# Optimization experiments

Measured on AMD Instinct MI355X. Metric: run time of the kernel, lower is better.

The kernel has to match this reference:

```python
import jax, jax.numpy as jnp
import numpy as np

B, S, D = 2, 2048, 2048          # batch, seq_len, model_dim
H, HD, RD, L = 16, 128, 64, 512  # heads, head_dim, rope_dim, latent_dim


def _rope_cos_sin(seq_len, dim, dtype):
    inv_freq = 1.0 / (10000.0 ** (jnp.arange(0, dim, 2, dtype=jnp.float32) / dim))
    freqs = jnp.outer(jnp.arange(seq_len, dtype=jnp.float32), inv_freq)  # [S, dim/2]
    emb = jnp.concatenate([freqs, freqs], axis=-1)                        # [S, dim]
    return jnp.cos(emb).astype(dtype), jnp.sin(emb).astype(dtype)


def _rotate_half(x):
    x1, x2 = jnp.split(x, 2, axis=-1)
    return jnp.concatenate([-x2, x1], axis=-1)


def _apply_rope(q, k):
    # q, k: [B, S, H, rope_dim]
    cos, sin = _rope_cos_sin(q.shape[1], q.shape[-1], q.dtype)
    cos = cos[None, :, None, :]
    sin = sin[None, :, None, :]
    return q * cos + _rotate_half(q) * sin, k * cos + _rotate_half(k) * sin


def setup_inputs() -> dict:
    key = jax.random.key(0)
    ks = jax.random.split(key, 6)
    x = jax.random.normal(ks[0], (B, S, D), dtype=jnp.float32)
    mask = jnp.tril(jnp.ones((1, 1, S, S), dtype=jnp.bool_))  # causal
    s = lambda fan_in: 1.0 / np.sqrt(fan_in)
    w_kv_down = jax.random.normal(ks[1], (D, L), jnp.float32) * s(D)
    w_kv_up = jax.random.normal(ks[2], (L, H * (2 * HD + RD)), jnp.float32) * s(L)
    w_q_down = jax.random.normal(ks[3], (D, L), jnp.float32) * s(D)
    w_q_up = jax.random.normal(ks[4], (L, H * (HD + RD)), jnp.float32) * s(L)
    w_o = jax.random.normal(ks[5], (H * HD, D), jnp.float32) * s(H * HD)
    return dict(x=x, mask=mask, w_kv_down=w_kv_down, w_kv_up=w_kv_up,
                w_q_down=w_q_down, w_q_up=w_q_up, w_o=w_o)


def reference(x, mask, w_kv_down, w_kv_up, w_q_down, w_q_up, w_o):
    b, s, _ = x.shape
    # low-rank KV path
    kv_full = (x @ w_kv_down @ w_kv_up).reshape(b, s, H, 2 * HD + RD)
    k_content = kv_full[..., :HD]
    k_rope = kv_full[..., HD:HD + RD]
    v = kv_full[..., HD + RD:]                     # [b, s, H, HD]
    # low-rank Q path
    q_full = (x @ w_q_down @ w_q_up).reshape(b, s, H, HD + RD)
    q_content = q_full[..., :HD]
    q_rope = q_full[..., HD:]
    # partial RoPE on the rope slice only
    q_rope, k_rope = _apply_rope(q_rope, k_rope)
    q = jnp.concatenate([q_content, q_rope], axis=-1)  # [b, s, H, HD+RD]
    k = jnp.concatenate([k_content, k_rope], axis=-1)
    scale = 1.0 / np.sqrt(HD + RD)
    scores = jnp.einsum('bqhd,bkhd->bhqk', q, k) * scale
    scores = jnp.where(mask, scores, jnp.finfo(scores.dtype).min)
    attn = jax.nn.softmax(scores, axis=-1)          # dropout_p=0.0 -> identity
    context = jnp.einsum('bhqk,bkhd->bqhd', attn, v).reshape(b, s, H * HD)
    return context @ w_o
```

## Files before the change

### kernel.cpp

```cpp
#include <hip/hip_runtime.h>
#include <hip/hip_bf16.h>

#define B_ 2
#define S_ 2048
#define D_ 2048
#define H_ 16
#define HD_ 128
#define RD_ 64
#define L_ 512
#define BS_ (B_ * S_)
#define KVH 320
#define QH 192

typedef unsigned short u16;
typedef __bf16 bf16x8 __attribute__((ext_vector_type(8)));
typedef float f32x4 __attribute__((ext_vector_type(4)));
typedef float f32x16 __attribute__((ext_vector_type(16)));
typedef unsigned short us8 __attribute__((ext_vector_type(8)));
typedef unsigned short us4 __attribute__((ext_vector_type(4)));

#define MFMA16(A, B, C) __builtin_amdgcn_mfma_f32_16x16x32_bf16((A), (B), (C), 0, 0, 0)
#define MFMA32(A, B, C) __builtin_amdgcn_mfma_f32_32x32x16_bf16((A), (B), (C), 0, 0, 0)

__device__ __forceinline__ u16 f2bf(float f) {
    unsigned int u = __builtin_bit_cast(unsigned int, f);
    u += 0x7FFFu + ((u >> 16) & 1u);
    return (u16)(u >> 16);
}
__device__ __forceinline__ float bf2f(u16 u) {
    unsigned int x = ((unsigned int)u) << 16;
    return __builtin_bit_cast(float, x);
}
__device__ __forceinline__ void async16(const void* g, void* l) {
    __builtin_amdgcn_global_load_lds((void __attribute__((address_space(1)))*)g,
                                     (void __attribute__((address_space(3)))*)l, 16, 0, 0);
}
__device__ __forceinline__ int swz4(int row) { return (row + (row >> 2)) & 3; }
__device__ __forceinline__ unsigned int cvtpk_bf16(float lo, float hi) {
    unsigned int r;
    asm("v_cvt_pk_bf16_f32 %0, %1, %2" : "=v"(r) : "v"(lo), "v"(hi));
    return r;
}

__global__ __launch_bounds__(256) void conv_f32_bf16(const float* __restrict__ in,
                                                     u16* __restrict__ outp) {
    const int i = blockIdx.x * 256 + threadIdx.x;
    float4 v = *(const float4*)(in + (size_t)i * 4);
    us4 o; o[0] = f2bf(v.x); o[1] = f2bf(v.y); o[2] = f2bf(v.z); o[3] = f2bf(v.w);
    *(us4*)(outp + (size_t)i * 4) = o;
}

__global__ __launch_bounds__(256) void transpose_f32_bf16(const float* __restrict__ W,
                                                          u16* __restrict__ Wt,
                                                          int K, int N) {
    __shared__ float tile[32][33];
    const int t = threadIdx.x, tx = t & 31, ty = t >> 5;
    const int n0 = blockIdx.x * 32, k0 = blockIdx.y * 32;
#pragma unroll
    for (int r = 0; r < 4; r++)
        tile[ty + 8 * r][tx] = W[(size_t)(k0 + ty + 8 * r) * N + n0 + tx];
    __syncthreads();
#pragma unroll
    for (int r = 0; r < 4; r++)
        Wt[(size_t)(n0 + ty + 8 * r) * K + k0 + tx] = f2bf(tile[tx][ty + 8 * r]);
}

__global__ __launch_bounds__(256) void transpose_v(const u16* __restrict__ kvf,
                                                   u16* __restrict__ vtg) {
    __shared__ u16 tile[32][33];
    const int t = threadIdx.x, tx = t & 31, ty = t >> 5;
    const int bh = blockIdx.z, b = bh >> 4, h = bh & 15;
    const int s0 = blockIdx.x * 32, d0 = blockIdx.y * 32;
#pragma unroll
    for (int r = 0; r < 4; r++)
        tile[ty + 8 * r][tx] = kvf[(size_t)(b * S_ + s0 + ty + 8 * r) * (H_ * KVH) + h * KVH + QH + d0 + tx];
    __syncthreads();
#pragma unroll
    for (int r = 0; r < 4; r++)
        vtg[((size_t)bh * HD_ + d0 + ty + 8 * r) * S_ + s0 + tx] = tile[tx][ty + 8 * r];
}

__global__ __launch_bounds__(256) void rope_both(u16* __restrict__ qf,
                                                 u16* __restrict__ kvf) {
    const int idx = blockIdx.x * 256 + threadIdx.x;
    const int d = idx & 31;
    const int h = (idx >> 5) & (H_ - 1);
    const int s = (idx >> 9) & (S_ - 1);
    const int b = idx >> 20;
    const int stride = blockIdx.y ? KVH : QH;
    u16* buf = blockIdx.y ? kvf : qf;

    const float inv_freq = powf(10000.0f, -(float)d * (1.0f / 32.0f));
    const float ang = (float)s * inv_freq;
    const float c = cosf(ang), sn = sinf(ang);

    u16* p = buf + ((size_t)((b * S_ + s) * H_) + h) * stride + HD_ + d;
    const float x1 = bf2f(p[0]);
    const float x2 = bf2f(p[32]);
    p[0]  = f2bf(x1 * c - x2 * sn);
    p[32] = f2bf(x2 * c + x1 * sn);
}

template <int WM, int WN, int TM, int TN, bool OUT_F32>
__global__ __launch_bounds__(WM * WN * 64) void gemm_bf16(
    const u16* __restrict__ A, int lda,
    const u16* __restrict__ Bt, int ldb,
    void* __restrict__ Cv, int ldc, int K, float alpha) {
    constexpr int BMt = WM * TM * 16;
    constexpr int BNt = WN * TN * 16;
    constexpr int NW  = WM * WN;
    constexpr int CA  = BMt / 16;
    constexpr int CB  = BNt / 16;

    __shared__ u16 As[BMt * 32];
    __shared__ u16 Bs[BNt * 32];

    const int t = threadIdx.x, w = t >> 6, l = t & 63;
    const int quad = l >> 4, n16 = l & 15;
    const int wr = w / WN, wc = w % WN;
    const size_t m0 = (size_t)blockIdx.y * BMt;
    const size_t n0 = (size_t)blockIdx.x * BNt;
    const int rowc = l >> 2, sbp = l & 3;

    f32x4 acc[TM][TN];
#pragma unroll
    for (int i = 0; i < TM; i++)
#pragma unroll
        for (int j = 0; j < TN; j++) acc[i][j] = (f32x4){0.f, 0.f, 0.f, 0.f};

    for (int k0 = 0; k0 < K; k0 += 32) {
#pragma unroll
        for (int c = w; c < CA; c += NW) {
            const int row = c * 16 + rowc;
            const int colc = ((sbp - swz4(row)) & 3) * 8;
            async16(A + (m0 + row) * lda + k0 + colc, &As[c * 512 + l * 8]);
        }
#pragma unroll
        for (int c = w; c < CB; c += NW) {
            const int row = c * 16 + rowc;
            const int colc = ((sbp - swz4(row)) & 3) * 8;
            async16(Bt + (n0 + row) * ldb + k0 + colc, &Bs[c * 512 + l * 8]);
        }
        __syncthreads();

        bf16x8 af[TM], bfr[TN];
#pragma unroll
        for (int i = 0; i < TM; i++) {
            const int row = wr * TM * 16 + i * 16 + n16;
            af[i] = *(const bf16x8*)&As[row * 32 + ((quad + swz4(row)) & 3) * 8];
        }
#pragma unroll
        for (int j = 0; j < TN; j++) {
            const int row = wc * TN * 16 + j * 16 + n16;
            bfr[j] = *(const bf16x8*)&Bs[row * 32 + ((quad + swz4(row)) & 3) * 8];
        }
#pragma unroll
        for (int i = 0; i < TM; i++)
#pragma unroll
            for (int j = 0; j < TN; j++) acc[i][j] = MFMA16(af[i], bfr[j], acc[i][j]);
        __syncthreads();
    }

#pragma unroll
    for (int i = 0; i < TM; i++) {
#pragma unroll
        for (int j = 0; j < TN; j++) {
#pragma unroll
            for (int r = 0; r < 4; r++) {
                const size_t row = m0 + wr * TM * 16 + i * 16 + quad * 4 + r;
                const size_t col = n0 + wc * TN * 16 + j * 16 + n16;
                const float v = acc[i][j][r] * alpha;
                if (OUT_F32) ((float*)Cv)[row * ldc + col] = v;
                else         ((u16*)Cv)[row * ldc + col] = f2bf(v);
            }
        }
    }
}

__global__ __launch_bounds__(128, 2) void attn_mfma(const u16* __restrict__ qf,
                                                    const u16* __restrict__ kvf,
                                                    const u16* __restrict__ vtg,
                                                    u16* __restrict__ ctx) {
    __shared__ u16 Ks[2][3 * 32 * 64];
    __shared__ u16 Vs[128 * 32];

    const int t = threadIdx.x, w = t >> 6, lane = t & 63;
    const int l31 = lane & 31, hi = lane >> 5;

    const int wg = blockIdx.x;
    const int xcd = wg & 7, j = wg >> 3;
    const int bh = xcd + 8 * (j & 3);
    const int qt = 31 - (j >> 2);
    const int b = bh >> 4, h = bh & 15;
    const int Q0 = qt * 64;

    const u16* Kbase = kvf + (size_t)(b * S_) * (H_ * KVH) + h * KVH;
    const u16* Vbase = vtg + (size_t)bh * HD_ * S_;

    const int scol = ((lane & 7) ^ (lane >> 3)) * 8;
    const int krl  = lane >> 3;
    const int vrow = lane >> 2;
    const int vcol = ((lane & 3) ^ (vrow & 3)) * 8;

    int koff[12];
#pragma unroll
    for (int c = 0; c < 12; c++)
        koff[c] = (c >> 2) * 2048 + (((c & 3) * 16 + hi * 8) ^ ((l31 & 7) * 8));
    int voff[2][4];
#pragma unroll
    for (int s = 0; s < 2; s++)
#pragma unroll
        for (int dt = 0; dt < 4; dt++)
            voff[s][dt] = (dt * 32 + l31) * 32 + ((s * 16 + hi * 8) ^ ((l31 & 3) * 8));

    bf16x8 qfrag[12];
    {
        const u16* qr = qf + (size_t)(b * S_ + Q0 + w * 32 + l31) * (H_ * QH) + h * QH + hi * 8;
#pragma unroll
        for (int c = 0; c < 12; c++) qfrag[c] = *(const bf16x8*)(qr + c * 16);
    }
    asm volatile("" ::: "memory");

    f32x16 O[4];
#pragma unroll
    for (int i = 0; i < 4; i++)
#pragma unroll
        for (int r = 0; r < 16; r++) O[i][r] = 0.f;
    float lrun = 0.f;

    const int qg = Q0 + w * 32 + l31;
    const int qmaxw = Q0 + w * 32 + 31;
    const int nkt = 2 * qt + 2;

#define ISSUE_K(KT, BUF)                                                        \
    _Pragma("unroll")                                                           \
    for (int ch = w; ch < 12; ch += 2) {                                        \
        const int c3 = ch >> 2, kq = ch & 3;                                    \
        async16(Kbase + (size_t)((KT) * 32 + kq * 8 + krl) * (H_ * KVH)         \
                      + c3 * 64 + scol,                                         \
                &Ks[BUF][c3 * 2048 + kq * 512 + lane * 8]);                     \
    }
#define ISSUE_V(KT)                                                             \
    _Pragma("unroll")                                                           \
    for (int ch = w; ch < 8; ch += 2) {                                         \
        async16(Vbase + (size_t)(ch * 16 + vrow) * S_ + (KT) * 32 + vcol,       \
                &Vs[ch * 512 + lane * 8]);                                      \
    }

    ISSUE_K(0, 0);
    ISSUE_V(0);

    for (int kt = 0; kt < nkt; kt++) {
        const int cur = kt & 1;
        if (kt > 0) {
            asm volatile("s_barrier" ::: "memory");
            ISSUE_V(kt);
        }
        if (kt + 1 < nkt) {
            ISSUE_K(kt + 1, cur ^ 1);
            asm volatile("s_waitcnt vmcnt(10)" ::: "memory");
        } else {
            asm volatile("s_waitcnt vmcnt(4)" ::: "memory");
        }
        asm volatile("s_barrier" ::: "memory");

        const bool active = (kt * 32) <= qmaxw;
        bf16x8 pfrag[2];
        if (active) {
            f32x16 sA;
#pragma unroll
            for (int r = 0; r < 16; r++) sA[r] = 0.f;
            __builtin_amdgcn_s_setprio(1);
#pragma unroll
            for (int c = 0; c < 12; c++) {
                bf16x8 kf = *(const bf16x8*)&Ks[cur][koff[c] + l31 * 64];
                sA = MFMA32(kf, qfrag[c], sA);
            }
            __builtin_amdgcn_s_setprio(0);

            const bool diag = (kt * 32 + 31) > (Q0 + w * 32);
#pragma unroll
            for (int r = 0; r < 16; r++) {
                const int crow = (r & 3) + 8 * (r >> 2) + 4 * hi;
                float pa = exp2f(sA[r]);
                if (diag && (kt * 32 + crow > qg)) pa = 0.f;
                lrun += pa;
                sA[r] = pa;
            }

#pragma unroll
            for (int s = 0; s < 2; s++) {
                const int r0 = s * 8;
                unsigned int x0 = cvtpk_bf16(sA[r0 + 0], sA[r0 + 1]);
                unsigned int y0 = cvtpk_bf16(sA[r0 + 4], sA[r0 + 5]);
                unsigned int x1 = cvtpk_bf16(sA[r0 + 2], sA[r0 + 3]);
                unsigned int y1 = cvtpk_bf16(sA[r0 + 6], sA[r0 + 7]);
                asm volatile("v_permlane32_swap_b32 %0, %1" : "+v"(x0), "+v"(y0));
                asm volatile("v_permlane32_swap_b32 %0, %1" : "+v"(x1), "+v"(y1));
                union { unsigned int wv[4]; bf16x8 v; } u_;
                u_.wv[0] = x0; u_.wv[1] = x1; u_.wv[2] = y0; u_.wv[3] = y1;
                pfrag[s] = u_.v;
            }
        }

        if (kt + 1 < nkt) asm volatile("s_waitcnt vmcnt(6)" ::: "memory");
        else              asm volatile("s_waitcnt vmcnt(0)" ::: "memory");
        asm volatile("s_barrier" ::: "memory");

        if (active) {
            __builtin_amdgcn_s_setprio(1);
#pragma unroll
            for (int s = 0; s < 2; s++) {
#pragma unroll
                for (int dt = 0; dt < 4; dt++) {
                    bf16x8 vf = *(const bf16x8*)&Vs[voff[s][dt]];
                    O[dt] = MFMA32(pfrag[s], vf, O[dt]);
                }
            }
            __builtin_amdgcn_s_setprio(0);
        }
    }
#undef ISSUE_K
#undef ISSUE_V

    lrun += __shfl_xor(lrun, 32, 64);
    float inv_[16];
#pragma unroll
    for (int r = 0; r < 16; r++) {
        const int crow = (r & 3) + 8 * (r >> 2) + 4 * hi;
        inv_[r] = 1.0f / __shfl(lrun, crow, 64);
    }
#pragma unroll
    for (int dt = 0; dt < 4; dt++)
#pragma unroll
        for (int r = 0; r < 16; r++) {
            const int crow = (r & 3) + 8 * (r >> 2) + 4 * hi;
            const int qrow = Q0 + w * 32 + crow;
            ctx[(size_t)(b * S_ + qrow) * (H_ * HD_) + h * HD_ + dt * 32 + l31] =
                f2bf(O[dt][r] * inv_[r]);
        }
}

extern "C" void kernel_launch(void* const* d_in, const int* in_sizes, int n_in,
                              void* d_out, int out_size, void* d_ws, size_t ws_size,
                              hipStream_t stream) {
    const float* x         = (const float*)d_in[0];
    const float* w_kv_down = (const float*)d_in[2];
    const float* w_kv_up   = (const float*)d_in[3];
    const float* w_q_down  = (const float*)d_in[4];
    const float* w_q_up    = (const float*)d_in[5];
    const float* w_o       = (const float*)d_in[6];
    float* out = (float*)d_out;

    char* ws = (char*)d_ws;
    size_t off = 0;
    u16* xb      = (u16*)(ws + off); off += (size_t)BS_ * D_ * 2;
    u16* wdt     = (u16*)(ws + off); off += (size_t)1024 * D_ * 2;
    u16* wkvup_t = (u16*)(ws + off); off += (size_t)(H_ * KVH) * L_ * 2;
    u16* wqup_t  = (u16*)(ws + off); off += (size_t)(H_ * QH) * L_ * 2;
    u16* wo_t    = (u16*)(ws + off); off += (size_t)D_ * (H_ * HD_) * 2;
    u16* low     = (u16*)(ws + off); off += (size_t)BS_ * 1024 * 2;
    u16* kv_full = (u16*)(ws + off); off += (size_t)BS_ * H_ * KVH * 2;
    u16* q_full  = (u16*)(ws + off); off += (size_t)BS_ * H_ * QH * 2;
    u16* vtg     = (u16*)(ws + off); off += (size_t)B_ * H_ * HD_ * S_ * 2;
    u16* ctx     = (u16*)(ws + off); off += (size_t)BS_ * H_ * HD_ * 2;

    const float qscale = 1.442695041f / 13.856406461f;

    conv_f32_bf16<<<(BS_ * D_) / 1024, 256, 0, stream>>>(x, xb);
    transpose_f32_bf16<<<dim3(L_ / 32, D_ / 32), 256, 0, stream>>>(w_kv_down, wdt, D_, L_);
    transpose_f32_bf16<<<dim3(L_ / 32, D_ / 32), 256, 0, stream>>>(w_q_down, wdt + (size_t)512 * D_, D_, L_);
    transpose_f32_bf16<<<dim3((H_ * KVH) / 32, L_ / 32), 256, 0, stream>>>(w_kv_up, wkvup_t, L_, H_ * KVH);
    transpose_f32_bf16<<<dim3((H_ * QH) / 32, L_ / 32), 256, 0, stream>>>(w_q_up, wqup_t, L_, H_ * QH);
    transpose_f32_bf16<<<dim3(D_ / 32, (H_ * HD_) / 32), 256, 0, stream>>>(w_o, wo_t, H_ * HD_, D_);

    gemm_bf16<2, 2, 4, 2, false><<<dim3(1024 / 64, BS_ / 128), 256, 0, stream>>>(
        xb, D_, wdt, D_, low, 1024, D_, 1.0f);
    gemm_bf16<2, 2, 4, 4, false><<<dim3((H_ * KVH) / 128, BS_ / 128), 256, 0, stream>>>(
        low, 1024, wkvup_t, L_, kv_full, H_ * KVH, L_, 1.0f);
    gemm_bf16<2, 2, 4, 4, false><<<dim3((H_ * QH) / 128, BS_ / 128), 256, 0, stream>>>(
        low + 512, 1024, wqup_t, L_, q_full, H_ * QH, L_, qscale);

    rope_both<<<dim3((B_ * S_ * H_ * 32) / 256, 2), 256, 0, stream>>>(q_full, kv_full);

    transpose_v<<<dim3(S_ / 32, HD_ / 32, B_ * H_), 256, 0, stream>>>(kv_full, vtg);

    attn_mfma<<<dim3(1024), 128, 0, stream>>>(q_full, kv_full, vtg, ctx);

    gemm_bf16<2, 2, 4, 4, true><<<dim3(D_ / 128, BS_ / 128), 256, 0, stream>>>(
        ctx, D_, wo_t, D_, out, D_, D_, 1.0f);
}
```

Before: 416.6 us.

## Enlarge attention tiles to 128 queries with split-K waves and LDS reduction

The attention kernel now uses 512-thread workgroups that each cover 128 query rows and 64-key tiles. Two groups of four waves split each key tile into halves, and their partial outputs and row sums are combined through shared memory at the end. This increases K/V reuse per block and changes the ordering of query tiles to balance causal work. The cost is more shared memory, extra barriers and a final reduction, and half the waves are idle during the epilogue.

```diff
diff --git a/kernel.cpp b/kernel.cpp
--- a/kernel.cpp
+++ b/kernel.cpp
@@ -177,45 +177,47 @@
     }
 }
 
-__global__ __launch_bounds__(128, 2) void attn_mfma(const u16* __restrict__ qf,
+__global__ __launch_bounds__(512, 1) void attn_mfma(const u16* __restrict__ qf,
                                                     const u16* __restrict__ kvf,
                                                     const u16* __restrict__ vtg,
                                                     u16* __restrict__ ctx) {
-    __shared__ u16 Ks[2][3 * 32 * 64];
-    __shared__ u16 Vs[128 * 32];
+    __shared__ u16 Ks[2][3 * 64 * 64];
+    __shared__ u16 Vs[128 * 64];
 
     const int t = threadIdx.x, w = t >> 6, lane = t & 63;
+    const int w4 = w & 3, half = w >> 2;
     const int l31 = lane & 31, hi = lane >> 5;
 
     const int wg = blockIdx.x;
-    const int xcd = wg & 7, j = wg >> 3;
-    const int bh = xcd + 8 * (j & 3);
-    const int qt = 31 - (j >> 2);
+    const int xcd = wg & 7, ii = wg >> 3;
+    const int tt = ii & 15;
+    const int pp = (tt & 1) ? (tt >> 1) : (15 - (tt >> 1));
+    const int qi = (ii & 32) ? (15 - pp) : pp;
+    const int bh = xcd + 8 * (ii >> 4);
     const int b = bh >> 4, h = bh & 15;
-    const int Q0 = qt * 64;
+    const int Q0 = qi * 128;
 
     const u16* Kbase = kvf + (size_t)(b * S_) * (H_ * KVH) + h * KVH;
     const u16* Vbase = vtg + (size_t)bh * HD_ * S_;
 
     const int scol = ((lane & 7) ^ (lane >> 3)) * 8;
     const int krl  = lane >> 3;
-    const int vrow = lane >> 2;
-    const int vcol = ((lane & 3) ^ (vrow & 3)) * 8;
 
     int koff[12];
 #pragma unroll
     for (int c = 0; c < 12; c++)
-        koff[c] = (c >> 2) * 2048 + (((c & 3) * 16 + hi * 8) ^ ((l31 & 7) * 8));
+        koff[c] = (c >> 2) * 4096 + (((c & 3) * 16 + hi * 8) ^ ((l31 & 7) * 8));
     int voff[2][4];
 #pragma unroll
-    for (int s = 0; s < 2; s++)
+    for (int sl = 0; sl < 2; sl++)
 #pragma unroll
         for (int dt = 0; dt < 4; dt++)
-            voff[s][dt] = (dt * 32 + l31) * 32 + ((s * 16 + hi * 8) ^ ((l31 & 3) * 8));
+            voff[sl][dt] = (dt * 32 + l31) * 64 +
+                           (((2 * half + sl) * 16 + hi * 8) ^ ((l31 & 7) * 8));
 
     bf16x8 qfrag[12];
     {
-        const u16* qr = qf + (size_t)(b * S_ + Q0 + w * 32 + l31) * (H_ * QH) + h * QH + hi * 8;
+        const u16* qr = qf + (size_t)(b * S_ + Q0 + w4 * 32 + l31) * (H_ * QH) + h * QH + hi * 8;
 #pragma unroll
         for (int c = 0; c < 12; c++) qfrag[c] = *(const bf16x8*)(qr + c * 16);
     }
@@ -228,22 +230,22 @@
         for (int r = 0; r < 16; r++) O[i][r] = 0.f;
     float lrun = 0.f;
 
-    const int qg = Q0 + w * 32 + l31;
-    const int qmaxw = Q0 + w * 32 + 31;
-    const int nkt = 2 * qt + 2;
+    const int qg = Q0 + w4 * 32 + l31;
+    const int qmaxw = Q0 + w4 * 32 + 31;
+    const int nkt = 2 * qi + 2;
 
 #define ISSUE_K(KT, BUF)                                                        \
     _Pragma("unroll")                                                           \
-    for (int ch = w; ch < 12; ch += 2) {                                        \
-        const int c3 = ch >> 2, kq = ch & 3;                                    \
-        async16(Kbase + (size_t)((KT) * 32 + kq * 8 + krl) * (H_ * KVH)         \
+    for (int ch = w; ch < 24; ch += 8) {                                        \
+        const int c3 = ch >> 3, kq = ch & 7;                                    \
+        async16(Kbase + (size_t)((KT) * 64 + kq * 8 + krl) * (H_ * KVH)         \
                       + c3 * 64 + scol,                                         \
-                &Ks[BUF][c3 * 2048 + kq * 512 + lane * 8]);                     \
+                &Ks[BUF][c3 * 4096 + kq * 512 + lane * 8]);                     \
     }
 #define ISSUE_V(KT)                                                             \
     _Pragma("unroll")                                                           \
-    for (int ch = w; ch < 8; ch += 2) {                                         \
-        async16(Vbase + (size_t)(ch * 16 + vrow) * S_ + (KT) * 32 + vcol,       \
+    for (int ch = w; ch < 16; ch += 8) {                                        \
+        async16(Vbase + (size_t)(ch * 8 + krl) * S_ + (KT) * 64 + scol,         \
                 &Vs[ch * 512 + lane * 8]);                                      \
     }
 
@@ -258,14 +260,15 @@
         }
         if (kt + 1 < nkt) {
             ISSUE_K(kt + 1, cur ^ 1);
-            asm volatile("s_waitcnt vmcnt(10)" ::: "memory");
+            asm volatile("s_waitcnt vmcnt(5)" ::: "memory");
         } else {
-            asm volatile("s_waitcnt vmcnt(4)" ::: "memory");
+            asm volatile("s_waitcnt vmcnt(2)" ::: "memory");
         }
         asm volatile("s_barrier" ::: "memory");
 
-        const bool active = (kt * 32) <= qmaxw;
-        bf16x8 pfrag[2];
+        const int kb0 = kt * 64 + 32 * half;
+        const bool active = kb0 <= qmaxw;
+        bf16x8 pfrag0, pfrag1;
         if (active) {
             f32x16 sA;
 #pragma unroll
@@ -273,49 +276,57 @@
             __builtin_amdgcn_s_setprio(1);
 #pragma unroll
             for (int c = 0; c < 12; c++) {
-                bf16x8 kf = *(const bf16x8*)&Ks[cur][koff[c] + l31 * 64];
+                bf16x8 kf = *(const bf16x8*)&Ks[cur][koff[c] + (half * 32 + l31) * 64];
                 sA = MFMA32(kf, qfrag[c], sA);
             }
             __builtin_amdgcn_s_setprio(0);
 
-            const bool diag = (kt * 32 + 31) > (Q0 + w * 32);
+            const bool diag = (kb0 + 31) > (Q0 + w4 * 32);
 #pragma unroll
             for (int r = 0; r < 16; r++) {
                 const int crow = (r & 3) + 8 * (r >> 2) + 4 * hi;
                 float pa = exp2f(sA[r]);
-                if (diag && (kt * 32 + crow > qg)) pa = 0.f;
+                if (diag && (kb0 + crow > qg)) pa = 0.f;
                 lrun += pa;
                 sA[r] = pa;
             }
 
-#pragma unroll
-            for (int s = 0; s < 2; s++) {
-                const int r0 = s * 8;
-                unsigned int x0 = cvtpk_bf16(sA[r0 + 0], sA[r0 + 1]);
-                unsigned int y0 = cvtpk_bf16(sA[r0 + 4], sA[r0 + 5]);
-                unsigned int x1 = cvtpk_bf16(sA[r0 + 2], sA[r0 + 3]);
-                unsigned int y1 = cvtpk_bf16(sA[r0 + 6], sA[r0 + 7]);
+            {
+                unsigned int x0 = cvtpk_bf16(sA[0], sA[1]);
+                unsigned int y0 = cvtpk_bf16(sA[4], sA[5]);
+                unsigned int x1 = cvtpk_bf16(sA[2], sA[3]);
+                unsigned int y1 = cvtpk_bf16(sA[6], sA[7]);
                 asm volatile("v_permlane32_swap_b32 %0, %1" : "+v"(x0), "+v"(y0));
                 asm volatile("v_permlane32_swap_b32 %0, %1" : "+v"(x1), "+v"(y1));
                 union { unsigned int wv[4]; bf16x8 v; } u_;
                 u_.wv[0] = x0; u_.wv[1] = x1; u_.wv[2] = y0; u_.wv[3] = y1;
-                pfrag[s] = u_.v;
-            }
-        }
-
-        if (kt + 1 < nkt) asm volatile("s_waitcnt vmcnt(6)" ::: "memory");
+                pfrag0 = u_.v;
+            }
+            {
+                unsigned int x0 = cvtpk_bf16(sA[8], sA[9]);
+                unsigned int y0 = cvtpk_bf16(sA[12], sA[13]);
+                unsigned int x1 = cvtpk_bf16(sA[10], sA[11]);
+                unsigned int y1 = cvtpk_bf16(sA[14], sA[15]);
+                asm volatile("v_permlane32_swap_b32 %0, %1" : "+v"(x0), "+v"(y0));
+                asm volatile("v_permlane32_swap_b32 %0, %1" : "+v"(x1), "+v"(y1));
+                union { unsigned int wv[4]; bf16x8 v; } u_;
+                u_.wv[0] = x0; u_.wv[1] = x1; u_.wv[2] = y0; u_.wv[3] = y1;
+                pfrag1 = u_.v;
+            }
+        }
+
+        if (kt + 1 < nkt) asm volatile("s_waitcnt vmcnt(3)" ::: "memory");
         else              asm volatile("s_waitcnt vmcnt(0)" ::: "memory");
         asm volatile("s_barrier" ::: "memory");
 
         if (active) {
             __builtin_amdgcn_s_setprio(1);
 #pragma unroll
-            for (int s = 0; s < 2; s++) {
-#pragma unroll
-                for (int dt = 0; dt < 4; dt++) {
-                    bf16x8 vf = *(const bf16x8*)&Vs[voff[s][dt]];
-                    O[dt] = MFMA32(pfrag[s], vf, O[dt]);
-                }
+            for (int dt = 0; dt < 4; dt++) {
+                bf16x8 vf0 = *(const bf16x8*)&Vs[voff[0][dt]];
+                O[dt] = MFMA32(pfrag0, vf0, O[dt]);
+                bf16x8 vf1 = *(const bf16x8*)&Vs[voff[1][dt]];
+                O[dt] = MFMA32(pfrag1, vf1, O[dt]);
             }
             __builtin_amdgcn_s_setprio(0);
         }
@@ -323,19 +334,38 @@
 #undef ISSUE_K
 #undef ISSUE_V
 
+    float* PS = (float*)&Ks[0][0];
     lrun += __shfl_xor(lrun, 32, 64);
+    if (half) PS[8192 + w4 * 32 + l31] = lrun;
+#pragma unroll
+    for (int dt = 0; dt < 4; dt++) {
+        if (half) {
+#pragma unroll
+            for (int r = 0; r < 16; r++) PS[w4 * 1024 + lane * 16 + r] = O[dt][r];
+        }
+        __syncthreads();
+        if (!half) {
+#pragma unroll
+            for (int r = 0; r < 16; r++) O[dt][r] += PS[w4 * 1024 + lane * 16 + r];
+        }
+        __syncthreads();
+    }
+    if (half) return;
+
+    const float ltot = lrun + PS[8192 + w4 * 32 + l31];
+
     float inv_[16];
 #pragma unroll
     for (int r = 0; r < 16; r++) {
         const int crow = (r & 3) + 8 * (r >> 2) + 4 * hi;
-        inv_[r] = 1.0f / __shfl(lrun, crow, 64);
+        inv_[r] = 1.0f / __shfl(ltot, crow, 64);
     }
 #pragma unroll
     for (int dt = 0; dt < 4; dt++)
 #pragma unroll
         for (int r = 0; r < 16; r++) {
             const int crow = (r & 3) + 8 * (r >> 2) + 4 * hi;
-            const int qrow = Q0 + w * 32 + crow;
+            const int qrow = Q0 + w4 * 32 + crow;
             ctx[(size_t)(b * S_ + qrow) * (H_ * HD_) + h * HD_ + dt * 32 + l31] =
                 f2bf(O[dt][r] * inv_[r]);
         }
@@ -385,7 +415,7 @@
 
     transpose_v<<<dim3(S_ / 32, HD_ / 32, B_ * H_), 256, 0, stream>>>(kv_full, vtg);
 
-    attn_mfma<<<dim3(1024), 128, 0, stream>>>(q_full, kv_full, vtg, ctx);
+    attn_mfma<<<dim3(512), 512, 0, stream>>>(q_full, kv_full, vtg, ctx);
 
     gemm_bf16<2, 2, 4, 4, true><<<dim3(D_ / 128, BS_ / 128), 256, 0, stream>>>(
         ctx, D_, wo_t, D_, out, D_, D_, 1.0f);
```

Result: slower. 446.2 us (+7.1%).
